# Kernel optimization log

Measured on AMD Instinct MI355X. Metric: run time of the kernel, lower is better.

Reference implementation:

```python
import jax, jax.numpy as jnp
import numpy as np

N, E = 20000, 320000
IN_F, H, D = 1280, 4, 128
HD = H * D  # 512
NEG_SLOPE = 0.2


def setup_inputs() -> dict:
    key = jax.random.key(0)
    ks = jax.random.split(key, 16)
    feature = jax.random.normal(ks[0], (1, N, IN_F), dtype=jnp.float32)
    src = jax.random.randint(ks[1], (E,), 0, N, dtype=jnp.int32)
    dst = jnp.sort(jax.random.randint(ks[2], (E,), 0, N, dtype=jnp.int32))
    s1 = 1.0 / np.sqrt(IN_F)
    s2 = 1.0 / np.sqrt(HD)
    W1 = jax.random.normal(ks[3], (IN_F, HD), dtype=jnp.float32) * s1
    al1 = jax.random.normal(ks[4], (H, D), dtype=jnp.float32) * s2
    ar1 = jax.random.normal(ks[5], (H, D), dtype=jnp.float32) * s2
    b1 = jnp.zeros((HD,), dtype=jnp.float32)
    W2 = jax.random.normal(ks[6], (HD, HD), dtype=jnp.float32) * s2
    al2 = jax.random.normal(ks[7], (H, D), dtype=jnp.float32) * s2
    ar2 = jax.random.normal(ks[8], (H, D), dtype=jnp.float32) * s2
    b2 = jnp.zeros((HD,), dtype=jnp.float32)
    Wfc = jax.random.normal(ks[9], (HD, 64), dtype=jnp.float32) * s2
    bfc = jnp.zeros((64,), dtype=jnp.float32)
    return dict(feature=feature, src=src, dst=dst, W1=W1, al1=al1, ar1=ar1,
                b1=b1, W2=W2, al2=al2, ar2=ar2, b2=b2, Wfc=Wfc, bfc=bfc)


def gat_conv(x, src, dst, W, al, ar, b):
    # x: (N, F_in) -> (N, H, D). DGL GATConv math, negative_slope=0.2.
    h = (x @ W).reshape(N, H, D)
    el = jnp.sum(h * al, axis=-1)                       # (N, H)
    er = jnp.sum(h * ar, axis=-1)                       # (N, H)
    e = jax.nn.leaky_relu(el[src] + er[dst], NEG_SLOPE)  # (E, H)
    # edge softmax segmented by destination node
    m = jax.ops.segment_max(e, dst, num_segments=N, indices_are_sorted=True)
    ex = jnp.exp(e - m[dst])                            # (E, H)
    denom = jax.ops.segment_sum(ex, dst, num_segments=N, indices_are_sorted=True)
    alpha = ex / denom[dst]                             # (E, H)
    out = jax.ops.segment_sum(alpha[:, :, None] * h[src], dst,
                              num_segments=N, indices_are_sorted=True)  # (N,H,D)
    return out + b.reshape(H, D)


def reference(feature, src, dst, W1, al1, ar1, b1, W2, al2, ar2, b2, Wfc, bfc):
    x = feature[0]                                      # squeeze(0) -> (N, 1280)
    out = gat_conv(x, src, dst, W1, al1, ar1, b1)
    out = jax.nn.elu(out).reshape(N, HD)
    out = gat_conv(out, src, dst, W2, al2, ar2, b2)
    out = jax.nn.elu(out).reshape(N, HD)
    out = out @ Wfc + bfc                               # (N, 64)
    out = jax.nn.elu(out[None])                         # (1, N, 64)
    return out
```

## Files before the change

### kernel.cpp

```cpp
#include <hip/hip_runtime.h>
#include <hip/hip_bf16.h>
#include <math.h>

typedef __bf16 bf16_t;
typedef __bf16 bf16x8 __attribute__((ext_vector_type(8)));
typedef float f32x4 __attribute__((ext_vector_type(4)));

__device__ __forceinline__ void gload_lds16(const void* g, void* l) {
  __builtin_amdgcn_global_load_lds((const __attribute__((address_space(1))) void*)g,
                                   (__attribute__((address_space(3))) void*)l, 16, 0, 0);
}

__global__ void castk(const float* __restrict__ in, bf16_t* __restrict__ out, int n) {
  int i = (blockIdx.x * blockDim.x + threadIdx.x) * 8;
  if (i >= n) return;
  float4 a = *(const float4*)(in + i);
  float4 b = *(const float4*)(in + i + 4);
  bf16x8 o;
  o[0] = (bf16_t)a.x; o[1] = (bf16_t)a.y; o[2] = (bf16_t)a.z; o[3] = (bf16_t)a.w;
  o[4] = (bf16_t)b.x; o[5] = (bf16_t)b.y; o[6] = (bf16_t)b.z; o[7] = (bf16_t)b.w;
  *(bf16x8*)(out + i) = o;
}

__global__ void transk(const float* __restrict__ in, bf16_t* __restrict__ out,
                       int K, int N) {
  __shared__ float t[32][33];
  int n0 = blockIdx.x * 32, k0 = blockIdx.y * 32;
  int tx = threadIdx.x & 31, ty = threadIdx.x >> 5;
#pragma unroll
  for (int r = ty; r < 32; r += 8) t[r][tx] = in[(size_t)(k0 + r) * N + n0 + tx];
  __syncthreads();
#pragma unroll
  for (int r = ty; r < 32; r += 8)
    out[(size_t)(n0 + r) * K + k0 + tx] = (bf16_t)t[tx][r];
}

__global__ void rowoffk(const int* __restrict__ dst, int* __restrict__ ro, int N, int E) {
  int n = blockIdx.x * blockDim.x + threadIdx.x;
  if (n > N) return;
  if (n == N) { ro[N] = E; return; }
  int lo = 0, hi = E;
  while (lo < hi) { int mid = (lo + hi) >> 1; if (dst[mid] < n) lo = mid + 1; else hi = mid; }
  ro[n] = lo;
}

__global__ void elerk(const bf16_t* __restrict__ Hb, const float* __restrict__ al,
                      const float* __restrict__ ar, float* __restrict__ el,
                      float* __restrict__ er, int N) {
  int node = blockIdx.x * 4 + (threadIdx.x >> 6);
  int lane = threadIdx.x & 63;
  if (node >= N) return;
  bf16x8 v = *(const bf16x8*)(Hb + (size_t)node * 512 + lane * 8);
  int head = lane >> 4;
  int dbase = (lane & 15) * 8;
  float sl = 0.f, sr = 0.f;
#pragma unroll
  for (int t = 0; t < 8; t++) {
    float f = (float)v[t];
    sl += f * al[head * 128 + dbase + t];
    sr += f * ar[head * 128 + dbase + t];
  }
#pragma unroll
  for (int off = 1; off < 16; off <<= 1) {
    sl += __shfl_xor(sl, off);
    sr += __shfl_xor(sr, off);
  }
  if ((lane & 15) == 0) {
    el[node * 4 + head] = sl;
    er[node * 4 + head] = sr;
  }
}

__global__ void edgek(const float* __restrict__ el, const float* __restrict__ er,
                      const int* __restrict__ src, const int* __restrict__ dst,
                      float* __restrict__ pw, int E) {
  int e = blockIdx.x * blockDim.x + threadIdx.x;
  if (e >= E) return;
  int s = src[e], d = dst[e];
  float4 ev = *(const float4*)(el + (size_t)s * 4);
  float4 rv = *(const float4*)(er + (size_t)d * 4);
  float c;
  c = ev.x + rv.x; c = c >= 0.f ? c : 0.2f * c; pw[e] = __expf(c);
  c = ev.y + rv.y; c = c >= 0.f ? c : 0.2f * c; pw[(size_t)E + e] = __expf(c);
  c = ev.z + rv.z; c = c >= 0.f ? c : 0.2f * c; pw[(size_t)2 * E + e] = __expf(c);
  c = ev.w + rv.w; c = c >= 0.f ? c : 0.2f * c; pw[(size_t)3 * E + e] = __expf(c);
}

#define GK_NPB 32
__global__ __launch_bounds__(256) void gatherk(
    const bf16_t* __restrict__ Hb, const float* __restrict__ pw,
    const int* __restrict__ src, const int* __restrict__ ro,
    const float* __restrict__ bias, bf16_t* __restrict__ out, int N, int E) {
  const int slice = blockIdx.x & 7;
  const int group = blockIdx.x >> 3;
  const int w = threadIdx.x >> 6, lane = threadIdx.x & 63;
  const int g = lane >> 3;
  const int oct = lane & 7;
  const int head = slice >> 1;
  const float* __restrict__ ph = pw + (size_t)head * E;
  const int dimbase = slice * 64 + oct * 8;

  const int n = group * GK_NPB + w * 8 + g;
  const int e0 = ro[n], e1 = ro[n + 1];

  float acc[8] = {0.f, 0.f, 0.f, 0.f, 0.f, 0.f, 0.f, 0.f};
  float psum = 0.f;

  for (int eb = e0 & ~7; eb < e1; eb += 8) {
    const int4 sv0 = *(const int4*)(src + eb);
    const int4 sv1 = *(const int4*)(src + eb + 4);
    const float4 pv0 = *(const float4*)(ph + eb);
    const float4 pv1 = *(const float4*)(ph + eb + 4);
    int ss[8]; float pp[8];
    ss[0] = sv0.x; ss[1] = sv0.y; ss[2] = sv0.z; ss[3] = sv0.w;
    ss[4] = sv1.x; ss[5] = sv1.y; ss[6] = sv1.z; ss[7] = sv1.w;
    pp[0] = pv0.x; pp[1] = pv0.y; pp[2] = pv0.z; pp[3] = pv0.w;
    pp[4] = pv1.x; pp[5] = pv1.y; pp[6] = pv1.z; pp[7] = pv1.w;
#pragma unroll
    for (int j = 0; j < 8; j++) {
      const int e = eb + j;
      if (e < e0 || e >= e1) pp[j] = 0.f;
    }
    bf16x8 v[8];
#pragma unroll
    for (int j = 0; j < 8; j++)
      v[j] = *(const bf16x8*)(Hb + (size_t)ss[j] * 512 + dimbase);
#pragma unroll
    for (int j = 0; j < 8; j++) {
      psum += pp[j];
#pragma unroll
      for (int t = 0; t < 8; t++) acc[t] += pp[j] * (float)v[j][t];
    }
  }

  const float ih = psum > 0.f ? 1.0f / psum : 0.f;
  const float4 b0 = *(const float4*)(bias + dimbase);
  const float4 b1 = *(const float4*)(bias + dimbase + 4);
  bf16x8 o; float vv;
  vv = acc[0] * ih + b0.x; o[0] = (bf16_t)(vv > 0.f ? vv : expm1f(vv));
  vv = acc[1] * ih + b0.y; o[1] = (bf16_t)(vv > 0.f ? vv : expm1f(vv));
  vv = acc[2] * ih + b0.z; o[2] = (bf16_t)(vv > 0.f ? vv : expm1f(vv));
  vv = acc[3] * ih + b0.w; o[3] = (bf16_t)(vv > 0.f ? vv : expm1f(vv));
  vv = acc[4] * ih + b1.x; o[4] = (bf16_t)(vv > 0.f ? vv : expm1f(vv));
  vv = acc[5] * ih + b1.y; o[5] = (bf16_t)(vv > 0.f ? vv : expm1f(vv));
  vv = acc[6] * ih + b1.z; o[6] = (bf16_t)(vv > 0.f ? vv : expm1f(vv));
  vv = acc[7] * ih + b1.w; o[7] = (bf16_t)(vv > 0.f ? vv : expm1f(vv));
  *(bf16x8*)(out + (size_t)n * 512 + dimbase) = o;
}

template <int BM, int BN, int WM, int WN, int EPI>
__global__ __launch_bounds__(256) void gemm_bt(
    const bf16_t* __restrict__ A, const bf16_t* __restrict__ Bt,
    void* __restrict__ C, const float* __restrict__ bias,
    int M, int N, int K) {
  constexpr int BK = 64;
  constexpr int WTM = BM / WM, WTN = BN / WN;
  constexpr int MF = WTM / 16, NF = WTN / 16;

  __shared__ bf16_t sA[BM][BK];
  __shared__ bf16_t sB[BN][BK];

  const int tid = threadIdx.x;
  const int wid = tid >> 6, lane = tid & 63;
  const int wr = wid / WN, wc = wid % WN;

  const int nby = N / BN;
  const int nwg = gridDim.x;
  const int q = nwg >> 3, r = nwg & 7;
  const int xcd = blockIdx.x & 7, pos = blockIdx.x >> 3;
  const int wg = (xcd < r ? xcd * (q + 1) : r * (q + 1) + (xcd - r) * q) + pos;
  const int row0 = (wg / nby) * BM;
  const int col0 = (wg % nby) * BN;

  f32x4 acc[MF][NF];
#pragma unroll
  for (int i = 0; i < MF; i++)
#pragma unroll
    for (int j = 0; j < NF; j++) acc[i][j] = (f32x4){0.f, 0.f, 0.f, 0.f};

  const int b_r = lane >> 3, b_p = lane & 7;

  for (int k0 = 0; k0 < K; k0 += BK) {
#pragma unroll
    for (int j = 0; j < BM / 32; j++) {
      const int rj = (j * 4 + wid) * 8;
      const int row = rj + b_r;
      int grow = row0 + row; if (grow > M - 1) grow = M - 1;
      const int s = b_p ^ (row & 7);
      gload_lds16(A + (size_t)grow * K + k0 + s * 8, &sA[rj][0]);
    }
#pragma unroll
    for (int j = 0; j < BN / 32; j++) {
      const int rj = (j * 4 + wid) * 8;
      const int row = rj + b_r;
      const int s = b_p ^ (row & 7);
      gload_lds16(Bt + (size_t)(col0 + row) * K + k0 + s * 8, &sB[rj][0]);
    }
    __syncthreads();

#pragma unroll
    for (int kk = 0; kk < BK; kk += 32) {
      bf16x8 af[MF], bfr[NF];
#pragma unroll
      for (int i = 0; i < MF; i++) {
        const int row = wr * WTM + i * 16 + (lane & 15);
        const int s = kk / 8 + (lane >> 4);
        const int p = s ^ (row & 7);
        af[i] = *(const bf16x8*)&sA[row][p * 8];
      }
#pragma unroll
      for (int j = 0; j < NF; j++) {
        const int row = wc * WTN + j * 16 + (lane & 15);
        const int s = kk / 8 + (lane >> 4);
        const int p = s ^ (row & 7);
        bfr[j] = *(const bf16x8*)&sB[row][p * 8];
      }
#pragma unroll
      for (int i = 0; i < MF; i++)
#pragma unroll
        for (int j = 0; j < NF; j++)
          acc[i][j] = __builtin_amdgcn_mfma_f32_16x16x32_bf16(af[i], bfr[j], acc[i][j], 0, 0, 0);
    }
    __syncthreads();
  }

#pragma unroll
  for (int i = 0; i < MF; i++) {
#pragma unroll
    for (int j = 0; j < NF; j++) {
#pragma unroll
      for (int rr = 0; rr < 4; rr++) {
        int row = row0 + wr * WTM + i * 16 + (lane >> 4) * 4 + rr;
        int col = col0 + wc * WTN + j * 16 + (lane & 15);
        if (row < M) {
          float v = acc[i][j][rr];
          if constexpr (EPI == 0) {
            ((bf16_t*)C)[(size_t)row * N + col] = (bf16_t)v;
          } else {
            v += bias[col];
            v = v > 0.f ? v : expm1f(v);
            ((float*)C)[(size_t)row * N + col] = v;
          }
        }
      }
    }
  }
}

extern "C" void kernel_launch(void* const* d_in, const int* in_sizes, int n_in,
                              void* d_out, int out_size, void* d_ws, size_t ws_size,
                              hipStream_t stream) {
  const float* feature = (const float*)d_in[0];
  const int* src = (const int*)d_in[1];
  const int* dst = (const int*)d_in[2];
  const float* W1 = (const float*)d_in[3];
  const float* al1 = (const float*)d_in[4];
  const float* ar1 = (const float*)d_in[5];
  const float* b1 = (const float*)d_in[6];
  const float* W2 = (const float*)d_in[7];
  const float* al2 = (const float*)d_in[8];
  const float* ar2 = (const float*)d_in[9];
  const float* b2 = (const float*)d_in[10];
  const float* Wfc = (const float*)d_in[11];
  const float* bfc = (const float*)d_in[12];

  const int N = 20000, E = 320000, INF = 1280, HD = 512;

  char* ws = (char*)d_ws;
  size_t off = 0;
  auto alloc = [&](size_t bytes) {
    void* p = ws + off;
    off += (bytes + 255) & ~(size_t)255;
    return p;
  };
  bf16_t* Xb  = (bf16_t*)alloc((size_t)N * INF * 2);
  bf16_t* W1t = (bf16_t*)alloc((size_t)HD * INF * 2);
  bf16_t* W2t = (bf16_t*)alloc((size_t)HD * HD * 2);
  bf16_t* Wft = (bf16_t*)alloc((size_t)64 * HD * 2);
  bf16_t* Hb  = (bf16_t*)alloc((size_t)N * HD * 2);
  bf16_t* Xn  = (bf16_t*)alloc((size_t)N * HD * 2);
  float* el = (float*)alloc((size_t)N * 4 * 4);
  float* er = (float*)alloc((size_t)N * 4 * 4);
  float* pw = (float*)alloc((size_t)E * 4 * 4);
  int* ro = (int*)alloc((size_t)(N + 1) * 4);

  castk<<<(N * INF) / (256 * 8), 256, 0, stream>>>(feature, Xb, N * INF);
  {
    dim3 g(HD / 32, INF / 32);
    transk<<<g, 256, 0, stream>>>(W1, W1t, INF, HD);
  }
  {
    dim3 g(HD / 32, HD / 32);
    transk<<<g, 256, 0, stream>>>(W2, W2t, HD, HD);
  }
  {
    dim3 g(64 / 32, HD / 32);
    transk<<<g, 256, 0, stream>>>(Wfc, Wft, HD, 64);
  }
  rowoffk<<<(N + 1 + 255) / 256, 256, 0, stream>>>(dst, ro, N, E);

  const int nbx = (N + 127) / 128;
  const int gatherBlocks = (N / GK_NPB) * 8;
  const int edgeBlocks = (E + 255) / 256;

  gemm_bt<128, 128, 2, 2, 0><<<nbx * (HD / 128), 256, 0, stream>>>(
      Xb, W1t, Hb, nullptr, N, HD, INF);
  elerk<<<N / 4, 256, 0, stream>>>(Hb, al1, ar1, el, er, N);
  edgek<<<edgeBlocks, 256, 0, stream>>>(el, er, src, dst, pw, E);
  gatherk<<<gatherBlocks, 256, 0, stream>>>(Hb, pw, src, ro, b1, Xn, N, E);

  gemm_bt<128, 128, 2, 2, 0><<<nbx * (HD / 128), 256, 0, stream>>>(
      Xn, W2t, Hb, nullptr, N, HD, HD);
  elerk<<<N / 4, 256, 0, stream>>>(Hb, al2, ar2, el, er, N);
  edgek<<<edgeBlocks, 256, 0, stream>>>(el, er, src, dst, pw, E);
  gatherk<<<gatherBlocks, 256, 0, stream>>>(Hb, pw, src, ro, b2, Xn, N, E);

  gemm_bt<128, 64, 4, 1, 1><<<nbx, 256, 0, stream>>>(Xn, Wft, d_out, bfc, N, 64, HD);
}
```

Baseline: 206.6 us.

## Fuse el/er attention-logit computation into the GEMM epilogue with one head per wave

Removes the separate elerk kernel and computes per-node per-head el/er dot products inside the projection GEMM epilogue from the fp32 accumulators. The GEMM tile widens to 128x256 so each wave covers exactly one 128-wide head, which lets the reduction finish with intra-wave shuffles. This saves a kernel launch and a full re-read of the bf16 H matrix per layer. In exchange, doubling the accumulator tile raises register pressure and halves the grid size, which may hurt occupancy and load balance. el/er are also now computed from fp32 values rather than bf16-rounded ones.

```diff
diff --git a/kernel.cpp b/kernel.cpp
--- a/kernel.cpp
+++ b/kernel.cpp
@@ -42,33 +42,6 @@
   int lo = 0, hi = E;
   while (lo < hi) { int mid = (lo + hi) >> 1; if (dst[mid] < n) lo = mid + 1; else hi = mid; }
   ro[n] = lo;
-}
-
-__global__ void elerk(const bf16_t* __restrict__ Hb, const float* __restrict__ al,
-                      const float* __restrict__ ar, float* __restrict__ el,
-                      float* __restrict__ er, int N) {
-  int node = blockIdx.x * 4 + (threadIdx.x >> 6);
-  int lane = threadIdx.x & 63;
-  if (node >= N) return;
-  bf16x8 v = *(const bf16x8*)(Hb + (size_t)node * 512 + lane * 8);
-  int head = lane >> 4;
-  int dbase = (lane & 15) * 8;
-  float sl = 0.f, sr = 0.f;
-#pragma unroll
-  for (int t = 0; t < 8; t++) {
-    float f = (float)v[t];
-    sl += f * al[head * 128 + dbase + t];
-    sr += f * ar[head * 128 + dbase + t];
-  }
-#pragma unroll
-  for (int off = 1; off < 16; off <<= 1) {
-    sl += __shfl_xor(sl, off);
-    sr += __shfl_xor(sr, off);
-  }
-  if ((lane & 15) == 0) {
-    el[node * 4 + head] = sl;
-    er[node * 4 + head] = sr;
-  }
 }
 
 __global__ void edgek(const float* __restrict__ el, const float* __restrict__ er,
@@ -152,10 +125,13 @@
 __global__ __launch_bounds__(256) void gemm_bt(
     const bf16_t* __restrict__ A, const bf16_t* __restrict__ Bt,
     void* __restrict__ C, const float* __restrict__ bias,
+    const float* __restrict__ al, const float* __restrict__ ar,
+    float* __restrict__ el, float* __restrict__ er,
     int M, int N, int K) {
   constexpr int BK = 64;
   constexpr int WTM = BM / WM, WTN = BN / WN;
   constexpr int MF = WTM / 16, NF = WTN / 16;
+  static_assert(EPI != 2 || WTN == 128, "fused el/er needs one head per wave");
 
   __shared__ bf16_t sA[BM][BK];
   __shared__ bf16_t sB[BN][BK];
@@ -234,14 +210,61 @@
         int col = col0 + wc * WTN + j * 16 + (lane & 15);
         if (row < M) {
           float v = acc[i][j][rr];
-          if constexpr (EPI == 0) {
-            ((bf16_t*)C)[(size_t)row * N + col] = (bf16_t)v;
-          } else {
+          if constexpr (EPI == 1) {
             v += bias[col];
             v = v > 0.f ? v : expm1f(v);
             ((float*)C)[(size_t)row * N + col] = v;
+          } else {
+            ((bf16_t*)C)[(size_t)row * N + col] = (bf16_t)v;
           }
         }
+      }
+    }
+  }
+
+  if constexpr (EPI == 2) {
+    const int h = (col0 + wc * WTN) >> 7;
+    float alv[NF], arv[NF];
+#pragma unroll
+    for (int j = 0; j < NF; j++) {
+      const int d = j * 16 + (lane & 15);
+      alv[j] = al[h * 128 + d];
+      arv[j] = ar[h * 128 + d];
+    }
+    float tl[MF][4], tr[MF][4];
+#pragma unroll
+    for (int i = 0; i < MF; i++)
+#pragma unroll
+      for (int rr = 0; rr < 4; rr++) {
+        float sl = 0.f, sr2 = 0.f;
+#pragma unroll
+        for (int j = 0; j < NF; j++) {
+          sl  += acc[i][j][rr] * alv[j];
+          sr2 += acc[i][j][rr] * arv[j];
+        }
+        tl[i][rr] = sl; tr[i][rr] = sr2;
+      }
+#pragma unroll
+    for (int msk = 1; msk < 16; msk <<= 1)
+#pragma unroll
+      for (int i = 0; i < MF; i++)
+#pragma unroll
+        for (int rr = 0; rr < 4; rr++) {
+          tl[i][rr] += __shfl_xor(tl[i][rr], msk);
+          tr[i][rr] += __shfl_xor(tr[i][rr], msk);
+        }
+    float outl = 0.f, outr = 0.f;
+#pragma unroll
+    for (int i = 0; i < MF; i++)
+#pragma unroll
+      for (int rr = 0; rr < 4; rr++)
+        if ((lane & 15) == i * 4 + rr) { outl = tl[i][rr]; outr = tr[i][rr]; }
+    {
+      const int L = lane & 15;
+      const int row = row0 + wr * WTM + (L >> 2) * 16 + (lane >> 4) * 4 + (L & 3);
+      if (row < M) {
+        el[(size_t)row * 4 + h] = outl;
+        er[(size_t)row * 4 + h] = outr;
       }
     }
   }
@@ -303,17 +326,16 @@
   const int gatherBlocks = (N / GK_NPB) * 8;
   const int edgeBlocks = (E + 255) / 256;
 
-  gemm_bt<128, 128, 2, 2, 0><<<nbx * (HD / 128), 256, 0, stream>>>(
-      Xb, W1t, Hb, nullptr, N, HD, INF);
-  elerk<<<N / 4, 256, 0, stream>>>(Hb, al1, ar1, el, er, N);
+  gemm_bt<128, 256, 2, 2, 2><<<nbx * (HD / 256), 256, 0, stream>>>(
+      Xb, W1t, Hb, nullptr, al1, ar1, el, er, N, HD, INF);
   edgek<<<edgeBlocks, 256, 0, stream>>>(el, er, src, dst, pw, E);
   gatherk<<<gatherBlocks, 256, 0, stream>>>(Hb, pw, src, ro, b1, Xn, N, E);
 
-  gemm_bt<128, 128, 2, 2, 0><<<nbx * (HD / 128), 256, 0, stream>>>(
-      Xn, W2t, Hb, nullptr, N, HD, HD);
-  elerk<<<N / 4, 256, 0, stream>>>(Hb, al2, ar2, el, er, N);
+  gemm_bt<128, 256, 2, 2, 2><<<nbx * (HD / 256), 256, 0, stream>>>(
+      Xn, W2t, Hb, nullptr, al2, ar2, el, er, N, HD, HD);
   edgek<<<edgeBlocks, 256, 0, stream>>>(el, er, src, dst, pw, E);
   gatherk<<<gatherBlocks, 256, 0, stream>>>(Hb, pw, src, ro, b2, Xn, N, E);
 
-  gemm_bt<128, 64, 4, 1, 1><<<nbx, 256, 0, stream>>>(Xn, Wft, d_out, bfc, N, 64, HD);
-}
+  gemm_bt<128, 64, 4, 1, 1><<<nbx, 256, 0, stream>>>(
+      Xn, Wft, d_out, bfc, nullptr, nullptr, nullptr, nullptr, N, 64, HD);
+}
```

Result: slower. 264.8 us (+28.2%).
